# Performance work log

Hardware: AMD Instinct MI355X
Metric: run time of the kernel (lower is better)

## Reference

```python
import jax, jax.numpy as jnp
import numpy as np

B, F, V_IN = 8, 64, 163842  # icosahedron order 7
V_OUT, K = 40962, 7         # order 6, 1-ring (6 neighbors + self)


def setup_inputs() -> dict:
    key = jax.random.key(0)
    kx, ki = jax.random.split(key)
    x = jax.random.normal(kx, (B, F, V_IN), dtype=jnp.float32)
    neigh_indices = jax.random.randint(ki, (V_OUT, K), 0, V_IN, dtype=jnp.int64)
    return {"x": x, "neigh_indices": neigh_indices}


def reference(x, neigh_indices):
    # Gather fixed-size 1-ring neighborhoods: (B, F, V_OUT, K)
    gathered = x[:, :, neigh_indices]
    # Mean pooling over the neighborhood axis (pooling_type='mean')
    pooled = jnp.mean(gathered, axis=-1)  # (B, F, V_OUT)
    # Original returns (pooled, max_pool_indices=None); indices are None for mean.
    return pooled
```

## Files before the change

kernel.cpp:

```cpp
#include <hip/hip_runtime.h>


typedef float f4 __attribute__((ext_vector_type(4)));

constexpr int B = 8, F = 64, V_IN = 163842, V_OUT = 40962, K = 7;
constexpr int ROWS = B * F;
constexpr int RG   = 16;
constexpr int NG   = ROWS / RG;
constexpr int TPB  = 256;
constexpr int GPX  = NG / 8;
constexpr int CPB  = 256;
constexpr int IBX  = (V_IN + CPB - 1) / CPB;
constexpr int VPT  = 4;
constexpr int VPB2 = 64 * VPT;
constexpr int VB2  = (V_OUT + VPB2 - 1) / VPB2;
constexpr int BLOCKS2 = 8 * GPX * VB2;
constexpr size_t XI_BYTES = (size_t)NG * V_IN * 64;

__global__ __launch_bounds__(TPB) void icopool_interleave_lds(
    const float* __restrict__ x, f4* __restrict__ xI)
{
    __shared__ float tile[RG][CPB + 1];
    const int g  = blockIdx.y;
    const int c0 = blockIdx.x * CPB;
    const int t  = threadIdx.x;

    if (c0 + CPB <= V_IN) {
        #pragma unroll
        for (int it = 0; it < 4; ++it) {
            const int r  = it * 4 + (t >> 6);
            const int c4 = (t & 63) * 4;
            const f4 vv = *(const f4*)(x + (size_t)(g * RG + r) * V_IN + c0 + c4);
            tile[r][c4 + 0] = vv.x;
            tile[r][c4 + 1] = vv.y;
            tile[r][c4 + 2] = vv.z;
            tile[r][c4 + 3] = vv.w;
        }
    } else {
        for (int it = 0; it < 4; ++it) {
            const int r  = it * 4 + (t >> 6);
            const int c4 = (t & 63) * 4;
            for (int jj = 0; jj < 4; ++jj) {
                const int c = c0 + c4 + jj;
                tile[r][c4 + jj] = (c < V_IN) ? x[(size_t)(g * RG + r) * V_IN + c] : 0.0f;
            }
        }
    }
    __syncthreads();

    f4* dst = xI + (size_t)g * V_IN * 4;
    #pragma unroll
    for (int it = 0; it < 4; ++it) {
        const int e = it * 64 + (t >> 2);
        const int q = t & 3;
        const int c = c0 + e;
        if (c < V_IN) {
            const f4 vv = { tile[q * 4 + 0][e], tile[q * 4 + 1][e],
                            tile[q * 4 + 2][e], tile[q * 4 + 3][e] };
            __builtin_nontemporal_store(vv, dst + (size_t)c * 4 + q);
        }
    }
}

__global__ __launch_bounds__(TPB) void icopool_gather16v(
    const f4* __restrict__ xI,
    const int* __restrict__ nidx,
    float*     __restrict__ out)
{
    const int b   = blockIdx.x;
    const int xcd = b & 7;
    const int j   = b >> 3;
    const int gl  = j / VB2;
    const int vb  = j % VB2;
    const int sub = threadIdx.x & 3;
    const int lv  = threadIdx.x >> 2;
    const int g   = xcd * GPX + gl;
    const f4* s   = xI + (size_t)g * V_IN * 4 + sub;

    #pragma unroll
    for (int i = 0; i < VPT; ++i) {
        const int v = vb * VPB2 + i * 64 + lv;
        if (v < V_OUT) {
            const int base = v * K;
            const int i0 = nidx[base + 0];
            const int i1 = nidx[base + 1];
            const int i2 = nidx[base + 2];
            const int i3 = nidx[base + 3];
            const int i4 = nidx[base + 4];
            const int i5 = nidx[base + 5];
            const int i6 = nidx[base + 6];
            f4 acc = s[(size_t)i0 * 4];
            acc += s[(size_t)i1 * 4];
            acc += s[(size_t)i2 * 4];
            acc += s[(size_t)i3 * 4];
            acc += s[(size_t)i4 * 4];
            acc += s[(size_t)i5 * 4];
            acc += s[(size_t)i6 * 4];
            acc *= (1.0f / 7.0f);
            float* o = out + (size_t)(g * RG + sub * 4) * V_OUT + v;
            __builtin_nontemporal_store(acc.x, o);
            __builtin_nontemporal_store(acc.y, o + (size_t)V_OUT);
            __builtin_nontemporal_store(acc.z, o + 2 * (size_t)V_OUT);
            __builtin_nontemporal_store(acc.w, o + 3 * (size_t)V_OUT);
        }
    }
}

constexpr int RPB  = 2;
constexpr int RGS  = ROWS / RPB;
constexpr int RG_PER_XCD = RGS / 8;
constexpr int VB1  = (V_OUT + TPB - 1) / TPB;
constexpr int BLOCKS_V1  = RGS * VB1;

__global__ __launch_bounds__(TPB) void icopool_gather(
    const float* __restrict__ x,
    const int*   __restrict__ nidx,
    float*       __restrict__ out)
{
    const int b        = blockIdx.x;
    const int xcd      = b & 7;
    const int j        = b >> 3;
    const int rg_local = j / VB1;
    const int vb       = j % VB1;
    const int rg       = xcd * RG_PER_XCD + rg_local;
    const int r0       = rg * RPB;

    const int v = vb * TPB + threadIdx.x;
    if (v >= V_OUT) return;

    const int base = v * K;
    const int i0 = nidx[base + 0];
    const int i1 = nidx[base + 1];
    const int i2 = nidx[base + 2];
    const int i3 = nidx[base + 3];
    const int i4 = nidx[base + 4];
    const int i5 = nidx[base + 5];
    const int i6 = nidx[base + 6];

    #pragma unroll
    for (int r = 0; r < RPB; ++r) {
        const float* xr = x + (size_t)(r0 + r) * V_IN;
        float sum = xr[i0] + xr[i1] + xr[i2] + xr[i3] + xr[i4] + xr[i5] + xr[i6];
        __builtin_nontemporal_store(sum * (1.0f / 7.0f),
                                    out + (size_t)(r0 + r) * V_OUT + v);
    }
}

extern "C" void kernel_launch(void* const* d_in, const int* in_sizes, int n_in,
                              void* d_out, int out_size, void* d_ws, size_t ws_size,
                              hipStream_t stream) {
    const float* x    = (const float*)d_in[0];
    const int*   nidx = (const int*)d_in[1];
    float*       out  = (float*)d_out;

    if (ws_size >= XI_BYTES && d_ws != nullptr) {
        f4* xI = (f4*)d_ws;
        icopool_interleave_lds<<<dim3(IBX, NG), dim3(TPB), 0, stream>>>(x, xI);
        icopool_gather16v<<<dim3(BLOCKS2), dim3(TPB), 0, stream>>>(xI, nidx, out);
    } else {
        icopool_gather<<<dim3(BLOCKS_V1), dim3(TPB), 0, stream>>>(x, nidx, out);
    }
}
```

Measured before the change: 652.5 us.

## Pack input into fp16 32-row interleaved layout before gathering

```diff
diff --git a/kernel.cpp b/kernel.cpp
--- a/kernel.cpp
+++ b/kernel.cpp
@@ -1,109 +1,114 @@
 #include <hip/hip_runtime.h>
 
 
-typedef float f4 __attribute__((ext_vector_type(4)));
+typedef float    f4 __attribute__((ext_vector_type(4)));
+typedef float    f8 __attribute__((ext_vector_type(8)));
+typedef _Float16 h8 __attribute__((ext_vector_type(8)));
+typedef unsigned int u4 __attribute__((ext_vector_type(4)));
 
 constexpr int B = 8, F = 64, V_IN = 163842, V_OUT = 40962, K = 7;
 constexpr int ROWS = B * F;
-constexpr int RG   = 16;
+constexpr int RG   = 32;
 constexpr int NG   = ROWS / RG;
 constexpr int TPB  = 256;
 constexpr int GPX  = NG / 8;
-constexpr int CPB  = 256;
+constexpr int CPB  = 128;
 constexpr int IBX  = (V_IN + CPB - 1) / CPB;
-constexpr int VPT  = 4;
-constexpr int VPB2 = 64 * VPT;
-constexpr int VB2  = (V_OUT + VPB2 - 1) / VPB2;
-constexpr int BLOCKS2 = 8 * GPX * VB2;
-constexpr size_t XI_BYTES = (size_t)NG * V_IN * 64;
+constexpr int LSH  = 34;
+constexpr int VPB  = 64;
+constexpr int VB   = (V_OUT + VPB - 1) / VPB;
+constexpr int BLOCKS2 = 8 * GPX * VB;
+constexpr size_t XH_BYTES = (size_t)NG * V_IN * 64;
 
-__global__ __launch_bounds__(TPB) void icopool_interleave_lds(
-    const float* __restrict__ x, f4* __restrict__ xI)
+__global__ __launch_bounds__(TPB) void icopool_pack_h(
+    const float* __restrict__ x, u4* __restrict__ xH)
 {
-    __shared__ float tile[RG][CPB + 1];
+    __shared__ _Float16 tile[CPB * LSH];
     const int g  = blockIdx.y;
     const int c0 = blockIdx.x * CPB;
     const int t  = threadIdx.x;
+    const int r  = t >> 3;
+    const int ci = t & 7;
 
+    const float* xr = x + (size_t)(g * RG + r) * V_IN;
     if (c0 + CPB <= V_IN) {
         #pragma unroll
         for (int it = 0; it < 4; ++it) {
-            const int r  = it * 4 + (t >> 6);
-            const int c4 = (t & 63) * 4;
-            const f4 vv = *(const f4*)(x + (size_t)(g * RG + r) * V_IN + c0 + c4);
-            tile[r][c4 + 0] = vv.x;
-            tile[r][c4 + 1] = vv.y;
-            tile[r][c4 + 2] = vv.z;
-            tile[r][c4 + 3] = vv.w;
+            const int c4 = ci * 4 + it * 32;
+            const f4 vv = *(const f4*)(xr + c0 + c4);
+            tile[(c4 + 0) * LSH + r] = (_Float16)vv.x;
+            tile[(c4 + 1) * LSH + r] = (_Float16)vv.y;
+            tile[(c4 + 2) * LSH + r] = (_Float16)vv.z;
+            tile[(c4 + 3) * LSH + r] = (_Float16)vv.w;
         }
     } else {
         for (int it = 0; it < 4; ++it) {
-            const int r  = it * 4 + (t >> 6);
-            const int c4 = (t & 63) * 4;
+            const int c4 = ci * 4 + it * 32;
             for (int jj = 0; jj < 4; ++jj) {
                 const int c = c0 + c4 + jj;
-                tile[r][c4 + jj] = (c < V_IN) ? x[(size_t)(g * RG + r) * V_IN + c] : 0.0f;
+                tile[(c4 + jj) * LSH + r] =
+                    (c < V_IN) ? (_Float16)xr[c] : (_Float16)0.0f;
             }
         }
     }
     __syncthreads();
 
-    f4* dst = xI + (size_t)g * V_IN * 4;
+    const unsigned int* ld = (const unsigned int*)tile;
+    u4* dst = xH + ((size_t)g * V_IN + c0) * 4;
     #pragma unroll
-    for (int it = 0; it < 4; ++it) {
-        const int e = it * 64 + (t >> 2);
-        const int q = t & 3;
-        const int c = c0 + e;
-        if (c < V_IN) {
-            const f4 vv = { tile[q * 4 + 0][e], tile[q * 4 + 1][e],
-                            tile[q * 4 + 2][e], tile[q * 4 + 3][e] };
-            __builtin_nontemporal_store(vv, dst + (size_t)c * 4 + q);
+    for (int it = 0; it < 2; ++it) {
+        const int c   = (t >> 2) + it * 64;
+        const int sub = t & 3;
+        if (c0 + c < V_IN) {
+            u4 w;
+            w.x = ld[c * 17 + sub * 4 + 0];
+            w.y = ld[c * 17 + sub * 4 + 1];
+            w.z = ld[c * 17 + sub * 4 + 2];
+            w.w = ld[c * 17 + sub * 4 + 3];
+            __builtin_nontemporal_store(w, dst + (size_t)c * 4 + sub);
         }
     }
 }
 
-__global__ __launch_bounds__(TPB) void icopool_gather16v(
-    const f4* __restrict__ xI,
+__global__ __launch_bounds__(TPB) void icopool_gather_h(
+    const h8* __restrict__ xH,
     const int* __restrict__ nidx,
     float*     __restrict__ out)
 {
     const int b   = blockIdx.x;
     const int xcd = b & 7;
     const int j   = b >> 3;
-    const int gl  = j / VB2;
-    const int vb  = j % VB2;
+    const int gl  = j / VB;
+    const int vb  = j % VB;
     const int sub = threadIdx.x & 3;
     const int lv  = threadIdx.x >> 2;
+    const int v   = vb * VPB + lv;
+    if (v >= V_OUT) return;
     const int g   = xcd * GPX + gl;
-    const f4* s   = xI + (size_t)g * V_IN * 4 + sub;
 
+    const int base = v * K;
+    const int i0 = nidx[base + 0];
+    const int i1 = nidx[base + 1];
+    const int i2 = nidx[base + 2];
+    const int i3 = nidx[base + 3];
+    const int i4 = nidx[base + 4];
+    const int i5 = nidx[base + 5];
+    const int i6 = nidx[base + 6];
+
+    const h8* s = xH + ((size_t)g * V_IN) * 4 + sub;
+    f8 acc = __builtin_convertvector(s[(size_t)i0 * 4], f8);
+    acc += __builtin_convertvector(s[(size_t)i1 * 4], f8);
+    acc += __builtin_convertvector(s[(size_t)i2 * 4], f8);
+    acc += __builtin_convertvector(s[(size_t)i3 * 4], f8);
+    acc += __builtin_convertvector(s[(size_t)i4 * 4], f8);
+    acc += __builtin_convertvector(s[(size_t)i5 * 4], f8);
+    acc += __builtin_convertvector(s[(size_t)i6 * 4], f8);
+    acc *= (1.0f / 7.0f);
+
+    float* o = out + (size_t)(g * RG + sub * 8) * V_OUT + v;
     #pragma unroll
-    for (int i = 0; i < VPT; ++i) {
-        const int v = vb * VPB2 + i * 64 + lv;
-        if (v < V_OUT) {
-            const int base = v * K;
-            const int i0 = nidx[base + 0];
-            const int i1 = nidx[base + 1];
-            const int i2 = nidx[base + 2];
-            const int i3 = nidx[base + 3];
-            const int i4 = nidx[base + 4];
-            const int i5 = nidx[base + 5];
-            const int i6 = nidx[base + 6];
-            f4 acc = s[(size_t)i0 * 4];
-            acc += s[(size_t)i1 * 4];
-            acc += s[(size_t)i2 * 4];
-            acc += s[(size_t)i3 * 4];
-            acc += s[(size_t)i4 * 4];
-            acc += s[(size_t)i5 * 4];
-            acc += s[(size_t)i6 * 4];
-            acc *= (1.0f / 7.0f);
-            float* o = out + (size_t)(g * RG + sub * 4) * V_OUT + v;
-            __builtin_nontemporal_store(acc.x, o);
-            __builtin_nontemporal_store(acc.y, o + (size_t)V_OUT);
-            __builtin_nontemporal_store(acc.z, o + 2 * (size_t)V_OUT);
-            __builtin_nontemporal_store(acc.w, o + 3 * (size_t)V_OUT);
-        }
-    }
+    for (int rr = 0; rr < 8; ++rr)
+        __builtin_nontemporal_store(acc[rr], o + (size_t)rr * V_OUT);
 }
 
 constexpr int RPB  = 2;
@@ -153,10 +158,10 @@
     const int*   nidx = (const int*)d_in[1];
     float*       out  = (float*)d_out;
 
-    if (ws_size >= XI_BYTES && d_ws != nullptr) {
-        f4* xI = (f4*)d_ws;
-        icopool_interleave_lds<<<dim3(IBX, NG), dim3(TPB), 0, stream>>>(x, xI);
-        icopool_gather16v<<<dim3(BLOCKS2), dim3(TPB), 0, stream>>>(xI, nidx, out);
+    if (ws_size >= XH_BYTES && d_ws != nullptr) {
+        u4* xH = (u4*)d_ws;
+        icopool_pack_h<<<dim3(IBX, NG), dim3(TPB), 0, stream>>>(x, xH);
+        icopool_gather_h<<<dim3(BLOCKS2), dim3(TPB), 0, stream>>>((const h8*)xH, nidx, out);
     } else {
         icopool_gather<<<dim3(BLOCKS_V1), dim3(TPB), 0, stream>>>(x, nidx, out);
     }
```

Result: faster. 578.8 us (-11.3%).
